# Kernel tuning notes

Hardware: AMD Instinct MI355X
Metric: run time of the kernel (lower is better)

## Reference

```python
import math
import jax, jax.numpy as jnp
import numpy as np

B, Q, HID = 4, 4, 4096
NH, NKV, HD = 32, 8, 128
GROUPS = NH // NKV
CACHE_LEN = 4096
CACHE_MAX = CACHE_LEN + 512  # prefill_len + max_len(512)
ROPE_THETA = 500000.0
SCALE = 1.0 / math.sqrt(128.0)  # hardcoded softmax_scale in module


def rotate_half(x):
    x1, x2 = jnp.split(x, 2, axis=-1)
    return jnp.concatenate([-x2, x1], axis=-1)


def setup_inputs() -> dict:
    key = jax.random.key(0)
    ks = jax.random.split(key, 8)
    std = 0.02
    # RoPE angles for positions [CACHE_LEN, CACHE_LEN+Q)
    pos = (CACHE_LEN + jnp.arange(Q)).astype(jnp.float32)
    inv_freq = 1.0 / (ROPE_THETA ** (jnp.arange(0, HD, 2, dtype=jnp.float32) / HD))
    freqs = pos[:, None] * inv_freq[None, :]            # [Q, HD/2]
    emb = jnp.concatenate([freqs, freqs], axis=-1)      # [Q, HD]
    cos = jnp.broadcast_to(jnp.cos(emb)[None], (B, Q, HD)).astype(jnp.float32)
    sin = jnp.broadcast_to(jnp.sin(emb)[None], (B, Q, HD)).astype(jnp.float32)
    return {
        "hidden_states": jax.random.normal(ks[0], (B, Q, HID), jnp.float32),
        "cos": cos,
        "sin": sin,
        "K_Cache": jax.random.normal(ks[1], (B, NKV, CACHE_MAX, HD), jnp.float32) * 0.5,
        "V_Cache": jax.random.normal(ks[2], (B, NKV, CACHE_MAX, HD), jnp.float32) * 0.5,
        "Wq": jax.random.normal(ks[3], (NH * HD, HID), jnp.float32) * std,
        "Wk": jax.random.normal(ks[4], (NKV * HD, HID), jnp.float32) * std,
        "Wv": jax.random.normal(ks[5], (NKV * HD, HID), jnp.float32) * std,
        "Wo": jax.random.normal(ks[6], (HID, NH * HD), jnp.float32) * std,
        "cache_lens": int(CACHE_LEN),
    }


def reference(hidden_states, cos, sin, K_Cache, V_Cache, Wq, Wk, Wv, Wo, cache_lens):
    b, q, _ = hidden_states.shape
    # projections (torch Linear: x @ W.T), reshape to [b, h, q, d]
    qs = jnp.einsum('bsh,oh->bso', hidden_states, Wq).reshape(b, q, NH, HD).transpose(0, 2, 1, 3)
    ks = jnp.einsum('bsh,oh->bso', hidden_states, Wk).reshape(b, q, NKV, HD).transpose(0, 2, 1, 3)
    vs = jnp.einsum('bsh,oh->bso', hidden_states, Wv).reshape(b, q, NKV, HD).transpose(0, 2, 1, 3)
    # RoPE, unsqueeze_dim=1 (head axis)
    c, s = cos[:, None, :, :], sin[:, None, :, :]
    qs = qs * c + rotate_half(qs) * s
    ks = ks * c + rotate_half(ks) * s
    # scatter new K/V into the cache at offset cache_lens
    K_Cache = K_Cache.at[:, :, cache_lens:cache_lens + q, :].set(ks)
    V_Cache = V_Cache.at[:, :, cache_lens:cache_lens + q, :].set(vs)
    # K_total/V_total = cache prefix ++ fresh keys/values; GQA repeat
    K_total = jnp.repeat(jnp.concatenate([K_Cache[:, :, :cache_lens, :], ks], axis=2), GROUPS, axis=1)
    V_total = jnp.repeat(jnp.concatenate([V_Cache[:, :, :cache_lens, :], vs], axis=2), GROUPS, axis=1)
    scores = jnp.einsum('bhqd,bhkd->bhqk', qs, K_total) * SCALE
    # causal mask over the appended q tokens, cache prefix fully visible
    tri = jnp.triu(jnp.ones((q, q), bool), 1)
    mask = jnp.concatenate([jnp.zeros((q, cache_lens), bool), tri], axis=1)
    scores = jnp.where(mask[None, None], -jnp.inf, scores)
    attn = jax.nn.softmax(scores.astype(jnp.float32), axis=-1).astype(V_total.dtype)
    out = jnp.einsum('bhqk,bhkd->bhqd', attn, V_total)
    out = out.transpose(0, 2, 1, 3).reshape(b, q, NH * HD)
    return jnp.einsum('bsh,oh->bso', out, Wo)
```

## Files before the change

kernel.cpp:

```cpp
#include <hip/hip_runtime.h>
#include <hip/hip_fp16.h>
#include <math.h>

#define HIDK 4096
#define NHQ 32
#define HD 128
#define CMAX 4608
#define CLEN 4096
#define NCH 32
#define SCALE 0.08838834764831845f

__device__ __forceinline__ float4 ld4(const float* p) { return *reinterpret_cast<const float4*>(p); }
__device__ __forceinline__ float dot4(float4 a, float4 b) { return a.x*b.x + a.y*b.y + a.z*b.z + a.w*b.w; }
__device__ __forceinline__ int kvidx(int pos, int dq) { return pos * 128 + (dq ^ ((pos & 7) << 2)); }

__global__ __launch_bounds__(256) void gemm3_kernel(
    const float* __restrict__ X,
    const float* __restrict__ W1, const float* __restrict__ W2, const float* __restrict__ W3,
    int n1, int n2,
    float* __restrict__ o1, int os1,
    float* __restrict__ o2, int os2,
    float* __restrict__ o3, int os3)
{
  __shared__ float Xs[2][16][256];

  const int tid = threadIdx.x, lane = tid & 63, w = tid >> 6;
  const int o = blockIdx.x * 8 + w * 2;

  const float* Wb; float* ob; int os;
  if (o < n1)           { Wb = W1 + (size_t)o * HIDK;            ob = o1 + o;            os = os1; }
  else if (o < n1 + n2) { const int f = o - n1;      Wb = W2 + (size_t)f * HIDK; ob = o2 + f; os = os2; }
  else                  { const int f = o - n1 - n2; Wb = W3 + (size_t)f * HIDK; ob = o3 + f; os = os3; }

  const int strow = tid >> 6;
  const int stcol = (tid & 63) * 4;

  float acc0[16], acc1[16];
  #pragma unroll
  for (int b = 0; b < 16; ++b) { acc0[b] = 0.f; acc1[b] = 0.f; }

  #pragma unroll
  for (int j = 0; j < 4; ++j)
    *(float4*)&Xs[0][strow + j * 4][stcol] = ld4(X + (size_t)(strow + j * 4) * HIDK + stcol);

  int cur = 0;
  #pragma unroll 2
  for (int kt = 0; kt < 16; ++kt) {
    const float4 w0 = ld4(Wb + (size_t)kt * 256 + lane * 4);
    const float4 w1 = ld4(Wb + HIDK + (size_t)kt * 256 + lane * 4);
    float4 g[4];
    if (kt < 15) {
      #pragma unroll
      for (int j = 0; j < 4; ++j)
        g[j] = ld4(X + (size_t)(strow + j * 4) * HIDK + (kt + 1) * 256 + stcol);
    }
    __syncthreads();
    #pragma unroll
    for (int b = 0; b < 16; ++b) {
      const float4 x4 = *(const float4*)&Xs[cur][b][lane * 4];
      acc0[b] += dot4(x4, w0);
      acc1[b] += dot4(x4, w1);
    }
    if (kt < 15) {
      #pragma unroll
      for (int j = 0; j < 4; ++j)
        *(float4*)&Xs[cur ^ 1][strow + j * 4][stcol] = g[j];
    }
    cur ^= 1;
  }

  #pragma unroll
  for (int m = 1; m < 64; m <<= 1)
    #pragma unroll
    for (int b = 0; b < 16; ++b) {
      acc0[b] += __shfl_xor(acc0[b], m, 64);
      acc1[b] += __shfl_xor(acc1[b], m, 64);
    }
  if (lane == 0) {
    #pragma unroll
    for (int b = 0; b < 16; ++b) {
      ob[(size_t)b * os]     = acc0[b];
      ob[(size_t)b * os + 1] = acc1[b];
    }
  }
}

__global__ __launch_bounds__(256) void qt_prep_kernel(
    const float* __restrict__ qraw, const float* __restrict__ cosp,
    const float* __restrict__ sinp, float* __restrict__ qt)
{
  const int e = blockIdx.x * 256 + threadIdx.x;
  const int d = e & 127;
  const int r = (e >> 7) & 15;
  const int bkv = e >> 11;
  const int b = bkv >> 3, kv = bkv & 7;
  const int s = r & 3, hl = r >> 2;
  const float* qp = qraw + (size_t)(b * 4 + s) * HIDK + (kv * 4 + hl) * HD;
  const float c  = cosp[(b * 4 + s) * HD + d];
  const float sn = sinp[(b * 4 + s) * HD + d];
  const float sgn = (d < 64) ? -1.f : 1.f;
  qt[e] = (qp[d] * c + sgn * qp[d ^ 64] * sn) * SCALE;
}

__global__ __launch_bounds__(128) void attn5_kernel(
    const float* __restrict__ qt, const float* __restrict__ Kc, const float* __restrict__ Vc,
    __half* __restrict__ partOh, float* __restrict__ partM, float* __restrict__ partL)
{
  __shared__ float qsh[16][128];
  __shared__ float KV[64 * 128];
  __shared__ float P[64][20];

  const int tid = threadIdx.x, lane = tid & 63, w = tid >> 6;
  const int chunk = blockIdx.x & 31, bkv = blockIdx.x >> 5;
  const int b = bkv >> 3, kv = bkv & 7;
  const int p0 = chunk * 128;

  const float* Kb = Kc + ((size_t)bkv * CMAX + p0) * HD;
  const float* Vb = Vc + ((size_t)bkv * CMAX + p0) * HD;

  const int dsub = tid & 31;
  const int rp   = tid >> 5;

  #pragma unroll
  for (int j = 0; j < 4; ++j) {
    const int fi = (tid + j * 128) * 4;
    *(float4*)&qsh[0][fi] = ld4(qt + (size_t)bkv * 2048 + fi);
  }
  #pragma unroll
  for (int i = 0; i < 16; ++i) {
    const int pos = i * 4 + rp;
    *(float4*)&KV[kvidx(pos, dsub * 4)] = ld4(Kb + (size_t)pos * HD + dsub * 4);
  }
  __syncthreads();

  float m[8], l[8];
  float4 o[8];
  #pragma unroll
  for (int r = 0; r < 8; ++r) { m[r] = -INFINITY; l[r] = 0.f; o[r] = make_float4(0.f, 0.f, 0.f, 0.f); }

  const int par = lane >> 5, dc = lane & 31;

  #pragma unroll
  for (int t = 0; t < 2; ++t) {
    float sc[8];
    #pragma unroll
    for (int r = 0; r < 8; ++r) sc[r] = 0.f;
    #pragma unroll 8
    for (int d4 = 0; d4 < 32; ++d4) {
      const float4 k4 = *(const float4*)&KV[kvidx(lane, d4 * 4)];
      #pragma unroll
      for (int r = 0; r < 8; ++r)
        sc[r] += dot4(k4, *(const float4*)&qsh[w * 8 + r][d4 * 4]);
    }
    #pragma unroll
    for (int r = 0; r < 8; ++r) {
      float mx = sc[r];
      #pragma unroll
      for (int st = 1; st < 64; st <<= 1) mx = fmaxf(mx, __shfl_xor(mx, st, 64));
      const float mn = fmaxf(m[r], mx);
      const float p  = __expf(sc[r] - mn);
      float ls = p;
      #pragma unroll
      for (int st = 1; st < 64; st <<= 1) ls += __shfl_xor(ls, st, 64);
      const float scal = __expf(m[r] - mn);
      m[r] = mn;
      l[r] = l[r] * scal + ls;
      o[r].x *= scal; o[r].y *= scal; o[r].z *= scal; o[r].w *= scal;
      P[lane][w * 8 + r] = p;
    }
    __syncthreads();
    #pragma unroll
    for (int i = 0; i < 16; ++i) {
      const int pos = i * 4 + rp;
      *(float4*)&KV[kvidx(pos, dsub * 4)] = ld4(Vb + (size_t)(t * 64 + pos) * HD + dsub * 4);
    }
    __syncthreads();
    #pragma unroll 8
    for (int i = 0; i < 32; ++i) {
      const int pos = 2 * i + par;
      const float4 v4 = *(const float4*)&KV[kvidx(pos, dc * 4)];
      const float4 pa = *(const float4*)&P[pos][w * 8];
      const float4 pb = *(const float4*)&P[pos][w * 8 + 4];
      o[0].x += pa.x * v4.x; o[0].y += pa.x * v4.y; o[0].z += pa.x * v4.z; o[0].w += pa.x * v4.w;
      o[1].x += pa.y * v4.x; o[1].y += pa.y * v4.y; o[1].z += pa.y * v4.z; o[1].w += pa.y * v4.w;
      o[2].x += pa.z * v4.x; o[2].y += pa.z * v4.y; o[2].z += pa.z * v4.z; o[2].w += pa.z * v4.w;
      o[3].x += pa.w * v4.x; o[3].y += pa.w * v4.y; o[3].z += pa.w * v4.z; o[3].w += pa.w * v4.w;
      o[4].x += pb.x * v4.x; o[4].y += pb.x * v4.y; o[4].z += pb.x * v4.z; o[4].w += pb.x * v4.w;
      o[5].x += pb.y * v4.x; o[5].y += pb.y * v4.y; o[5].z += pb.y * v4.z; o[5].w += pb.y * v4.w;
      o[6].x += pb.z * v4.x; o[6].y += pb.z * v4.y; o[6].z += pb.z * v4.z; o[6].w += pb.z * v4.w;
      o[7].x += pb.w * v4.x; o[7].y += pb.w * v4.y; o[7].z += pb.w * v4.z; o[7].w += pb.w * v4.w;
    }
    if (t == 0) {
      __syncthreads();
      #pragma unroll
      for (int i = 0; i < 16; ++i) {
        const int pos = i * 4 + rp;
        *(float4*)&KV[kvidx(pos, dsub * 4)] = ld4(Kb + (size_t)(64 + pos) * HD + dsub * 4);
      }
      __syncthreads();
    }
  }

  #pragma unroll
  for (int r = 0; r < 8; ++r) {
    o[r].x += __shfl_xor(o[r].x, 32, 64);
    o[r].y += __shfl_xor(o[r].y, 32, 64);
    o[r].z += __shfl_xor(o[r].z, 32, 64);
    o[r].w += __shfl_xor(o[r].w, 32, 64);
  }
  if (lane < 32) {
    #pragma unroll
    for (int r = 0; r < 8; ++r) {
      const int rg = w * 8 + r;
      const int hl = rg >> 2, s = rg & 3;
      const int row = (b * NHQ + kv * 4 + hl) * 4 + s;
      const size_t idx = ((size_t)row * NCH + chunk) * HD + dc * 4;
      *(__half2*)&partOh[idx]     = __floats2half2_rn(o[r].x, o[r].y);
      *(__half2*)&partOh[idx + 2] = __floats2half2_rn(o[r].z, o[r].w);
      if (dc == 0) {
        partM[row * NCH + chunk] = m[r];
        partL[row * NCH + chunk] = l[r];
      }
    }
  }
}

__global__ __launch_bounds__(64) void combine_kernel(
    const float* __restrict__ qt, const float* __restrict__ kraw, const float* __restrict__ vraw,
    const float* __restrict__ cosp, const float* __restrict__ sinp,
    const __half* __restrict__ partOh, const float* __restrict__ partM, const float* __restrict__ partL,
    float* __restrict__ attn)
{
  const int bid = blockIdx.x;
  const int s = bid & 3;
  const int h = (bid >> 2) & 31;
  const int b = bid >> 7;
  const int kv = h >> 2;
  const int lane = threadIdx.x;
  const int d0 = lane * 2;

  float M = -INFINITY;
  #pragma unroll 4
  for (int c = 0; c < NCH; ++c) M = fmaxf(M, partM[bid * NCH + c]);

  const int rloc = (h & 3) * 4 + s;
  const float qr0 = qt[((size_t)(b * 8 + kv) * 16 + rloc) * 128 + d0];
  const float qr1 = qt[((size_t)(b * 8 + kv) * 16 + rloc) * 128 + d0 + 1];

  float sj[4] = {0.f, 0.f, 0.f, 0.f};
  float Mp = M;
  #pragma unroll
  for (int j = 0; j < 4; ++j) {
    if (j <= s) {
      const float* kp = kraw + (size_t)(b * 4 + j) * 1024 + kv * HD;
      const float c0 = cosp[(b * 4 + j) * HD + d0],     sn0 = sinp[(b * 4 + j) * HD + d0];
      const float c1 = cosp[(b * 4 + j) * HD + d0 + 1], sn1 = sinp[(b * 4 + j) * HD + d0 + 1];
      const float sg0 = (d0 < 64) ? -1.f : 1.f;
      const float sg1 = ((d0 + 1) < 64) ? -1.f : 1.f;
      const float kr0 = kp[d0] * c0 + sg0 * kp[d0 ^ 64] * sn0;
      const float kr1 = kp[d0 + 1] * c1 + sg1 * kp[(d0 + 1) ^ 64] * sn1;
      float part = qr0 * kr0 + qr1 * kr1;
      #pragma unroll
      for (int m = 1; m < 64; m <<= 1) part += __shfl_xor(part, m, 64);
      sj[j] = part;
      Mp = fmaxf(Mp, part);
    }
  }

  float ltot = 0.f, O0 = 0.f, O1 = 0.f;
  #pragma unroll 4
  for (int c = 0; c < NCH; ++c) {
    const float a = __expf(partM[bid * NCH + c] - Mp);
    ltot += partL[bid * NCH + c] * a;
    const float2 v = __half22float2(*(const __half2*)&partOh[((size_t)bid * NCH + c) * HD + d0]);
    O0 += a * v.x;
    O1 += a * v.y;
  }
  #pragma unroll
  for (int j = 0; j < 4; ++j) {
    if (j <= s) {
      const float e = __expf(sj[j] - Mp);
      ltot += e;
      const float* vp = vraw + (size_t)(b * 4 + j) * 1024 + kv * HD + d0;
      O0 += e * vp[0];
      O1 += e * vp[1];
    }
  }
  const float inv = 1.f / ltot;
  *(float2*)&attn[(size_t)(b * 4 + s) * HIDK + h * HD + d0] = make_float2(O0 * inv, O1 * inv);
}

extern "C" void kernel_launch(void* const* d_in, const int* in_sizes, int n_in,
                              void* d_out, int out_size, void* d_ws, size_t ws_size,
                              hipStream_t stream)
{
  const float* hid  = (const float*)d_in[0];
  const float* cosp = (const float*)d_in[1];
  const float* sinp = (const float*)d_in[2];
  const float* Kc   = (const float*)d_in[3];
  const float* Vc   = (const float*)d_in[4];
  const float* Wq   = (const float*)d_in[5];
  const float* Wk   = (const float*)d_in[6];
  const float* Wv   = (const float*)d_in[7];
  const float* Wo   = (const float*)d_in[8];
  float* out = (float*)d_out;

  float* ws    = (float*)d_ws;
  float*  kraw   = ws;
  float*  vraw   = ws + 16384;
  float*  attn   = ws + 32768;
  float*  qt     = ws + 98304;
  float*  qraw   = ws + 163840;
  float*  partM  = ws + 229376;
  float*  partL  = ws + 245760;
  __half* partOh = (__half*)(ws + 262144);

  gemm3_kernel<<<768, 256, 0, stream>>>(hid, Wq, Wk, Wv, 4096, 1024,
                                        qraw, 4096, kraw, 1024, vraw, 1024);
  qt_prep_kernel<<<256, 256, 0, stream>>>(qraw, cosp, sinp, qt);
  attn5_kernel<<<1024, 128, 0, stream>>>(qt, Kc, Vc, partOh, partM, partL);
  combine_kernel<<<512, 64, 0, stream>>>(qt, kraw, vraw, cosp, sinp,
                                         partOh, partM, partL, attn);
  gemm3_kernel<<<512, 256, 0, stream>>>(attn, Wo, Wo, Wo, 4096, 0,
                                        out, 4096, out, 4096, out, 4096);
}
```

Measured before the change: 134.1 us.

## Prefetch weights four tiles ahead in GEMM and store K/V tiles as fp16 in LDS

The GEMM kernel keeps a four-deep register ring of weight float4 loads, so weight fetches are issued several iterations before they are used. The attention kernel now converts K and V tiles to half precision when writing them to shared memory, with a wider XOR swizzle. It also reads Q directly from global memory instead of staging it in shared memory. This cuts LDS footprint and bandwidth and may raise occupancy, but it costs extra register pressure and conversion instructions and loses precision on the cached K and V values.

New measurement: 174.3 us. +30.0%, slower.

```diff
diff --git a/kernel.cpp b/kernel.cpp
--- a/kernel.cpp
+++ b/kernel.cpp
@@ -12,9 +12,8 @@
 
 __device__ __forceinline__ float4 ld4(const float* p) { return *reinterpret_cast<const float4*>(p); }
 __device__ __forceinline__ float dot4(float4 a, float4 b) { return a.x*b.x + a.y*b.y + a.z*b.z + a.w*b.w; }
-__device__ __forceinline__ int kvidx(int pos, int dq) { return pos * 128 + (dq ^ ((pos & 7) << 2)); }
-
-__global__ __launch_bounds__(256) void gemm3_kernel(
+
+__global__ __launch_bounds__(256) void gemm4_kernel(
     const float* __restrict__ X,
     const float* __restrict__ W1, const float* __restrict__ W2, const float* __restrict__ W3,
     int n1, int n2,
@@ -43,11 +42,16 @@
   for (int j = 0; j < 4; ++j)
     *(float4*)&Xs[0][strow + j * 4][stcol] = ld4(X + (size_t)(strow + j * 4) * HIDK + stcol);
 
+  float4 wb0[4], wb1[4];
+  #pragma unroll
+  for (int s = 0; s < 4; ++s) {
+    wb0[s] = ld4(Wb + (size_t)s * 256 + lane * 4);
+    wb1[s] = ld4(Wb + HIDK + (size_t)s * 256 + lane * 4);
+  }
+
   int cur = 0;
-  #pragma unroll 2
+  #pragma unroll 4
   for (int kt = 0; kt < 16; ++kt) {
-    const float4 w0 = ld4(Wb + (size_t)kt * 256 + lane * 4);
-    const float4 w1 = ld4(Wb + HIDK + (size_t)kt * 256 + lane * 4);
     float4 g[4];
     if (kt < 15) {
       #pragma unroll
@@ -55,6 +59,12 @@
         g[j] = ld4(X + (size_t)(strow + j * 4) * HIDK + (kt + 1) * 256 + stcol);
     }
     __syncthreads();
+    const float4 w0 = wb0[kt & 3];
+    const float4 w1 = wb1[kt & 3];
+    if (kt < 12) {
+      wb0[kt & 3] = ld4(Wb + (size_t)(kt + 4) * 256 + lane * 4);
+      wb1[kt & 3] = ld4(Wb + HIDK + (size_t)(kt + 4) * 256 + lane * 4);
+    }
     #pragma unroll
     for (int b = 0; b < 16; ++b) {
       const float4 x4 = *(const float4*)&Xs[cur][b][lane * 4];
@@ -102,13 +112,14 @@
   qt[e] = (qp[d] * c + sgn * qp[d ^ 64] * sn) * SCALE;
 }
 
-__global__ __launch_bounds__(128) void attn5_kernel(
+__global__ __launch_bounds__(128) void attn6_kernel(
     const float* __restrict__ qt, const float* __restrict__ Kc, const float* __restrict__ Vc,
     __half* __restrict__ partOh, float* __restrict__ partM, float* __restrict__ partL)
 {
-  __shared__ float qsh[16][128];
-  __shared__ float KV[64 * 128];
-  __shared__ float P[64][20];
+  __shared__ float2 KVs[64 * 32];
+  __shared__ float  P[64][20];
+
+  __half* KV = (__half*)KVs;
 
   const int tid = threadIdx.x, lane = tid & 63, w = tid >> 6;
   const int chunk = blockIdx.x & 31, bkv = blockIdx.x >> 5;
@@ -117,21 +128,12 @@
 
   const float* Kb = Kc + ((size_t)bkv * CMAX + p0) * HD;
   const float* Vb = Vc + ((size_t)bkv * CMAX + p0) * HD;
-
-  const int dsub = tid & 31;
-  const int rp   = tid >> 5;
-
-  #pragma unroll
-  for (int j = 0; j < 4; ++j) {
-    const int fi = (tid + j * 128) * 4;
-    *(float4*)&qsh[0][fi] = ld4(qt + (size_t)bkv * 2048 + fi);
-  }
-  #pragma unroll
-  for (int i = 0; i < 16; ++i) {
-    const int pos = i * 4 + rp;
-    *(float4*)&KV[kvidx(pos, dsub * 4)] = ld4(Kb + (size_t)pos * HD + dsub * 4);
-  }
-  __syncthreads();
+  const float* qb = qt + (size_t)bkv * 2048 + (size_t)(w * 8) * 128;
+
+  const int sd = tid & 31;
+  const int sp = tid >> 5;
+
+  #define KVIDX(pos, d4) ((pos) * 128 + (((d4) * 4) ^ (((pos) & 31) << 2)))
 
   float m[8], l[8];
   float4 o[8];
@@ -139,6 +141,17 @@
   for (int r = 0; r < 8; ++r) { m[r] = -INFINITY; l[r] = 0.f; o[r] = make_float4(0.f, 0.f, 0.f, 0.f); }
 
   const int par = lane >> 5, dc = lane & 31;
+
+  #pragma unroll
+  for (int rr = 0; rr < 16; ++rr) {
+    const int pos = sp + rr * 4;
+    const float4 v = ld4(Kb + (size_t)pos * HD + sd * 4);
+    union { float2 f; __half2 h[2]; } u;
+    u.h[0] = __floats2half2_rn(v.x, v.y);
+    u.h[1] = __floats2half2_rn(v.z, v.w);
+    *(float2*)&KV[KVIDX(pos, sd)] = u.f;
+  }
+  __syncthreads();
 
   #pragma unroll
   for (int t = 0; t < 2; ++t) {
@@ -147,10 +160,15 @@
     for (int r = 0; r < 8; ++r) sc[r] = 0.f;
     #pragma unroll 8
     for (int d4 = 0; d4 < 32; ++d4) {
-      const float4 k4 = *(const float4*)&KV[kvidx(lane, d4 * 4)];
-      #pragma unroll
-      for (int r = 0; r < 8; ++r)
-        sc[r] += dot4(k4, *(const float4*)&qsh[w * 8 + r][d4 * 4]);
+      union { float2 f; __half2 h[2]; } u;
+      u.f = *(const float2*)&KV[KVIDX(lane, d4)];
+      const float2 kA = __half22float2(u.h[0]);
+      const float2 kB = __half22float2(u.h[1]);
+      #pragma unroll
+      for (int r = 0; r < 8; ++r) {
+        const float4 q4 = ld4(qb + r * 128 + d4 * 4);
+        sc[r] += kA.x * q4.x + kA.y * q4.y + kB.x * q4.z + kB.y * q4.w;
+      }
     }
     #pragma unroll
     for (int r = 0; r < 8; ++r) {
@@ -162,40 +180,51 @@
       float ls = p;
       #pragma unroll
       for (int st = 1; st < 64; st <<= 1) ls += __shfl_xor(ls, st, 64);
-      const float scal = __expf(m[r] - mn);
+      const float rs = __expf(m[r] - mn);
       m[r] = mn;
-      l[r] = l[r] * scal + ls;
-      o[r].x *= scal; o[r].y *= scal; o[r].z *= scal; o[r].w *= scal;
+      l[r] = l[r] * rs + ls;
+      o[r].x *= rs; o[r].y *= rs; o[r].z *= rs; o[r].w *= rs;
       P[lane][w * 8 + r] = p;
     }
     __syncthreads();
     #pragma unroll
-    for (int i = 0; i < 16; ++i) {
-      const int pos = i * 4 + rp;
-      *(float4*)&KV[kvidx(pos, dsub * 4)] = ld4(Vb + (size_t)(t * 64 + pos) * HD + dsub * 4);
+    for (int rr = 0; rr < 16; ++rr) {
+      const int pos = sp + rr * 4;
+      const float4 v = ld4(Vb + (size_t)(t * 64 + pos) * HD + sd * 4);
+      union { float2 f; __half2 h[2]; } u;
+      u.h[0] = __floats2half2_rn(v.x, v.y);
+      u.h[1] = __floats2half2_rn(v.z, v.w);
+      *(float2*)&KV[KVIDX(pos, sd)] = u.f;
     }
     __syncthreads();
     #pragma unroll 8
     for (int i = 0; i < 32; ++i) {
       const int pos = 2 * i + par;
-      const float4 v4 = *(const float4*)&KV[kvidx(pos, dc * 4)];
+      union { float2 f; __half2 h[2]; } u;
+      u.f = *(const float2*)&KV[KVIDX(pos, dc)];
+      const float2 vA = __half22float2(u.h[0]);
+      const float2 vB = __half22float2(u.h[1]);
       const float4 pa = *(const float4*)&P[pos][w * 8];
       const float4 pb = *(const float4*)&P[pos][w * 8 + 4];
-      o[0].x += pa.x * v4.x; o[0].y += pa.x * v4.y; o[0].z += pa.x * v4.z; o[0].w += pa.x * v4.w;
-      o[1].x += pa.y * v4.x; o[1].y += pa.y * v4.y; o[1].z += pa.y * v4.z; o[1].w += pa.y * v4.w;
-      o[2].x += pa.z * v4.x; o[2].y += pa.z * v4.y; o[2].z += pa.z * v4.z; o[2].w += pa.z * v4.w;
-      o[3].x += pa.w * v4.x; o[3].y += pa.w * v4.y; o[3].z += pa.w * v4.z; o[3].w += pa.w * v4.w;
-      o[4].x += pb.x * v4.x; o[4].y += pb.x * v4.y; o[4].z += pb.x * v4.z; o[4].w += pb.x * v4.w;
-      o[5].x += pb.y * v4.x; o[5].y += pb.y * v4.y; o[5].z += pb.y * v4.z; o[5].w += pb.y * v4.w;
-      o[6].x += pb.z * v4.x; o[6].y += pb.z * v4.y; o[6].z += pb.z * v4.z; o[6].w += pb.z * v4.w;
-      o[7].x += pb.w * v4.x; o[7].y += pb.w * v4.y; o[7].z += pb.w * v4.z; o[7].w += pb.w * v4.w;
+      o[0].x += pa.x * vA.x; o[0].y += pa.x * vA.y; o[0].z += pa.x * vB.x; o[0].w += pa.x * vB.y;
+      o[1].x += pa.y * vA.x; o[1].y += pa.y * vA.y; o[1].z += pa.y * vB.x; o[1].w += pa.y * vB.y;
+      o[2].x += pa.z * vA.x; o[2].y += pa.z * vA.y; o[2].z += pa.z * vB.x; o[2].w += pa.z * vB.y;
+      o[3].x += pa.w * vA.x; o[3].y += pa.w * vA.y; o[3].z += pa.w * vB.x; o[3].w += pa.w * vB.y;
+      o[4].x += pb.x * vA.x; o[4].y += pb.x * vA.y; o[4].z += pb.x * vB.x; o[4].w += pb.x * vB.y;
+      o[5].x += pb.y * vA.x; o[5].y += pb.y * vA.y; o[5].z += pb.y * vB.x; o[5].w += pb.y * vB.y;
+      o[6].x += pb.z * vA.x; o[6].y += pb.z * vA.y; o[6].z += pb.z * vB.x; o[6].w += pb.z * vB.y;
+      o[7].x += pb.w * vA.x; o[7].y += pb.w * vA.y; o[7].z += pb.w * vB.x; o[7].w += pb.w * vB.y;
     }
     if (t == 0) {
       __syncthreads();
       #pragma unroll
-      for (int i = 0; i < 16; ++i) {
-        const int pos = i * 4 + rp;
-        *(float4*)&KV[kvidx(pos, dsub * 4)] = ld4(Kb + (size_t)(64 + pos) * HD + dsub * 4);
+      for (int rr = 0; rr < 16; ++rr) {
+        const int pos = sp + rr * 4;
+        const float4 v = ld4(Kb + (size_t)(64 + pos) * HD + sd * 4);
+        union { float2 f; __half2 h[2]; } u;
+        u.h[0] = __floats2half2_rn(v.x, v.y);
+        u.h[1] = __floats2half2_rn(v.z, v.w);
+        *(float2*)&KV[KVIDX(pos, sd)] = u.f;
       }
       __syncthreads();
     }
@@ -223,6 +252,7 @@
       }
     }
   }
+  #undef KVIDX
 }
 
 __global__ __launch_bounds__(64) void combine_kernel(
@@ -315,12 +345,12 @@
   float*  partL  = ws + 245760;
   __half* partOh = (__half*)(ws + 262144);
 
-  gemm3_kernel<<<768, 256, 0, stream>>>(hid, Wq, Wk, Wv, 4096, 1024,
+  gemm4_kernel<<<768, 256, 0, stream>>>(hid, Wq, Wk, Wv, 4096, 1024,
                                         qraw, 4096, kraw, 1024, vraw, 1024);
   qt_prep_kernel<<<256, 256, 0, stream>>>(qraw, cosp, sinp, qt);
-  attn5_kernel<<<1024, 128, 0, stream>>>(qt, Kc, Vc, partOh, partM, partL);
+  attn6_kernel<<<1024, 128, 0, stream>>>(qt, Kc, Vc, partOh, partM, partL);
   combine_kernel<<<512, 64, 0, stream>>>(qt, kraw, vraw, cosp, sinp,
                                          partOh, partM, partL, attn);
-  gemm3_kernel<<<512, 256, 0, stream>>>(attn, Wo, Wo, Wo, 4096, 0,
+  gemm4_kernel<<<512, 256, 0, stream>>>(attn, Wo, Wo, Wo, 4096, 0,
                                         out, 4096, out, 4096, out, 4096);
 }
```
